# Kernel optimization log

Measured on AMD Instinct MI355X. Metric: run time of the kernel, lower is better.

The kernel has to match this reference:

```python
import jax, jax.numpy as jnp
import numpy as np

N_NODES = 50000
N_HEDGES = 10000
NNZ_INC = 400000
NNZ_E = 80000
NNZ_V = 400000
VDIM = 128
EDIM = 128
OUT_VDIM = 128
OUT_EDIM = 128


def _spmm(rows, cols, vals, X, n_rows):
    # sparse COO [n_rows, n_cols] @ X  -> [n_rows, d]
    return jax.ops.segment_sum(vals[:, None] * X[cols], rows, num_segments=n_rows)


def setup_inputs() -> dict:
    key = jax.random.key(0)
    ks = jax.random.split(key, 20)
    inp = {
        "vfeat": jax.random.normal(ks[0], (N_NODES, VDIM), jnp.float32),
        "efeat": jax.random.normal(ks[1], (N_HEDGES, EDIM), jnp.float32),
        "invDV": jax.random.uniform(ks[2], (N_NODES,), jnp.float32),
        "invDE": jax.random.uniform(ks[3], (N_HEDGES,), jnp.float32),
        "inc_src": jax.random.randint(ks[4], (NNZ_INC,), 0, N_NODES, jnp.int32),
        "inc_dst": jax.random.randint(ks[5], (NNZ_INC,), 0, N_HEDGES, jnp.int32),
        "emat_rows": jax.random.randint(ks[6], (NNZ_E,), 0, N_HEDGES, jnp.int32),
        "emat_cols": jax.random.randint(ks[7], (NNZ_E,), 0, N_HEDGES, jnp.int32),
        "emat_vals": jax.random.normal(ks[8], (NNZ_E,), jnp.float32),
        "vmat_rows": jax.random.randint(ks[9], (NNZ_V,), 0, N_NODES, jnp.int32),
        "vmat_cols": jax.random.randint(ks[10], (NNZ_V,), 0, N_NODES, jnp.int32),
        "vmat_vals": jax.random.normal(ks[11], (NNZ_V,), jnp.float32),
        # parameters (torch Linear: y = x @ W.T + b)
        "Wv": jax.random.normal(ks[12], (OUT_VDIM, VDIM), jnp.float32) * 0.05,
        "We": jax.random.normal(ks[13], (OUT_EDIM, EDIM), jnp.float32) * 0.05,
        "psi1_W": jax.random.normal(ks[14], (VDIM, VDIM + EDIM), jnp.float32) * 0.05,
        "psi1_b": jnp.zeros((VDIM,), jnp.float32),
        "psi2_W": jax.random.normal(ks[15], (EDIM, OUT_VDIM + EDIM), jnp.float32) * 0.05,
        "psi2_b": jnp.zeros((EDIM,), jnp.float32),
    }
    return inp


def reference(vfeat, efeat, invDV, invDE, inc_src, inc_dst,
              emat_rows, emat_cols, emat_vals,
              vmat_rows, vmat_cols, vmat_vals,
              Wv, We, psi1_W, psi1_b, psi2_W, psi2_b):
    N = vfeat.shape[0]
    E = efeat.shape[0]
    # --- 'in' update_all with psi1: per-incidence concat -> linear -> *invDV[src] -> sum into hyperedge
    x = jnp.concatenate([vfeat[inc_src], efeat[inc_dst]], axis=1)  # [nnz, VDIM+EDIM]
    x = x @ psi1_W.T + psi1_b                                       # [nnz, VDIM]
    x = x * invDV[inc_src][:, None]
    A = jax.ops.segment_sum(x, inc_dst, num_segments=E)             # [E, VDIM]
    A = _spmm(emat_rows, emat_cols, emat_vals, A, E)
    _efeat = A + efeat
    # --- 'con' update_all: node gathers sum of incident hyperedge feats
    _vfeat = jax.ops.segment_sum(_efeat[inc_dst], inc_src, num_segments=N)
    vfeat_out = jax.nn.relu(_vfeat @ Wv.T)                           # [N, OUT_VDIM]
    # --- 'in' update_all with psi2 (dv = ones)
    x2 = jnp.concatenate([vfeat_out[inc_src], efeat[inc_dst]], axis=1)
    x2 = x2 @ psi2_W.T + psi2_b                                      # [nnz, EDIM]
    B = jax.ops.segment_sum(x2, inc_dst, num_segments=E) * invDE[:, None]
    # --- 'con' pass with efeat, then vMat spmm, then 'in' sum back to hyperedges
    _vfeat2 = jax.ops.segment_sum(efeat[inc_dst], inc_src, num_segments=N)
    _vfeat2 = _spmm(vmat_rows, vmat_cols, vmat_vals, _vfeat2, N)
    _efeat2 = jax.ops.segment_sum(_vfeat2[inc_src], inc_dst, num_segments=E)
    _efeat2 = _efeat2 + B
    efeat_out = jax.nn.relu(_efeat2 @ We.T)                          # [E, OUT_EDIM]
    return vfeat_out, efeat_out
```

## Files before the change

### kernel.cpp

```cpp
#include <hip/hip_runtime.h>

#define NN 50000
#define NE 10000
#define NNZ_INC 400000
#define NNZ_E 80000
#define NNZ_V 400000
#define D 128
#define KC 32

#define CAP_D 112
#define CAP_S 40
#define CAP_E 40
#define CAP_V 40

#define NE_SH (NE / 8)
#define NN_SH (NN / 8)

#define GN_ 782
#define GE_ 157
#define G_HINC ((NNZ_INC + 255) / 256)
#define G_HIST8 (8 * G_HINC)
#define G_EV ((NNZ_E + NNZ_V + 255) / 256)
#define G_CVTN 6250
#define G_CVTE 1250
#define G_NR16 (NN / 16)
#define G_ER16 (NE / 16)

typedef unsigned short u16;
typedef unsigned int u32;

__device__ __forceinline__ u16 f2bf(float x) {
    unsigned u = __float_as_uint(x);
    unsigned r = u + 0x7fffu + ((u >> 16) & 1u);
    return (u16)(r >> 16);
}
__device__ __forceinline__ float bf2f(u16 h) {
    return __uint_as_float(((unsigned)h) << 16);
}

__device__ __forceinline__ void acc8(uint4 u, float acc[8]) {
    acc[0] += __uint_as_float(u.x << 16);
    acc[1] += __uint_as_float(u.x & 0xffff0000u);
    acc[2] += __uint_as_float(u.y << 16);
    acc[3] += __uint_as_float(u.y & 0xffff0000u);
    acc[4] += __uint_as_float(u.z << 16);
    acc[5] += __uint_as_float(u.z & 0xffff0000u);
    acc[6] += __uint_as_float(u.w << 16);
    acc[7] += __uint_as_float(u.w & 0xffff0000u);
}
__device__ __forceinline__ void fma8(uint4 u, float v, float acc[8]) {
    acc[0] = fmaf(v, __uint_as_float(u.x << 16), acc[0]);
    acc[1] = fmaf(v, __uint_as_float(u.x & 0xffff0000u), acc[1]);
    acc[2] = fmaf(v, __uint_as_float(u.y << 16), acc[2]);
    acc[3] = fmaf(v, __uint_as_float(u.y & 0xffff0000u), acc[3]);
    acc[4] = fmaf(v, __uint_as_float(u.z << 16), acc[4]);
    acc[5] = fmaf(v, __uint_as_float(u.z & 0xffff0000u), acc[5]);
    acc[6] = fmaf(v, __uint_as_float(u.w << 16), acc[6]);
    acc[7] = fmaf(v, __uint_as_float(u.w & 0xffff0000u), acc[7]);
}
__device__ __forceinline__ uint4 pack_bf8(const float acc[8]) {
    uint4 o;
    o.x = (u32)f2bf(acc[0]) | ((u32)f2bf(acc[1]) << 16);
    o.y = (u32)f2bf(acc[2]) | ((u32)f2bf(acc[3]) << 16);
    o.z = (u32)f2bf(acc[4]) | ((u32)f2bf(acc[5]) << 16);
    o.w = (u32)f2bf(acc[6]) | ((u32)f2bf(acc[7]) << 16);
    return o;
}

__device__ __forceinline__ void gemm_acc(
    int bx, const float* __restrict__ X, const float* __restrict__ W, int ldw,
    int M, float acc[8][4])
{
    __shared__ float XsT[KC][68];
    __shared__ float Ws[KC][132];
    const int tid = threadIdx.x;
    const int tx = tid & 31, ty = tid >> 5;
    const int row0 = bx * 64;
    const int c0 = tx * 4;
    const int r0 = ty * 8;

#pragma unroll
    for (int r = 0; r < 8; ++r)
#pragma unroll
        for (int c = 0; c < 4; ++c) acc[r][c] = 0.f;

    for (int kc = 0; kc < D; kc += KC) {
        __syncthreads();
#pragma unroll
        for (int it = 0; it < 2; ++it) {
            int l = tid + it * 256;
            int r = l >> 3, k4 = l & 7;
            float4 v = make_float4(0.f, 0.f, 0.f, 0.f);
            int row = row0 + r;
            if (row < M) v = ((const float4*)(X + (size_t)row * D + kc))[k4];
            int k = k4 * 4;
            XsT[k + 0][r] = v.x; XsT[k + 1][r] = v.y;
            XsT[k + 2][r] = v.z; XsT[k + 3][r] = v.w;
        }
#pragma unroll
        for (int it = 0; it < 4; ++it) {
            int l = tid + it * 256;
            int o = l >> 3, k4 = l & 7;
            float4 w = ((const float4*)(W + (size_t)o * ldw + kc))[k4];
            int k = k4 * 4;
            Ws[k + 0][o] = w.x; Ws[k + 1][o] = w.y;
            Ws[k + 2][o] = w.z; Ws[k + 3][o] = w.w;
        }
        __syncthreads();
#pragma unroll
        for (int k = 0; k < KC; ++k) {
            const float4 a0 = *(const float4*)&XsT[k][r0];
            const float4 a1 = *(const float4*)&XsT[k][r0 + 4];
            const float4 b  = *(const float4*)&Ws[k][c0];
            float av[8] = {a0.x, a0.y, a0.z, a0.w, a1.x, a1.y, a1.z, a1.w};
            float bv[4] = {b.x, b.y, b.z, b.w};
#pragma unroll
            for (int r = 0; r < 8; ++r)
#pragma unroll
                for (int c = 0; c < 4; ++c)
                    acc[r][c] = fmaf(av[r], bv[c], acc[r][c]);
        }
    }
}

__device__ __forceinline__ void gemm_acc2(
    int bx, const float* __restrict__ X1, const float* __restrict__ X2,
    const float* __restrict__ rsf,
    const float* __restrict__ W, int M, float acc[8][4])
{
    __shared__ float XsT[KC][68];
    __shared__ float Ws[KC][132];
    const int tid = threadIdx.x;
    const int tx = tid & 31, ty = tid >> 5;
    const int row0 = bx * 64;
    const int c0 = tx * 4;
    const int r0 = ty * 8;

#pragma unroll
    for (int r = 0; r < 8; ++r)
#pragma unroll
        for (int c = 0; c < 4; ++c) acc[r][c] = 0.f;

    for (int kc = 0; kc < 2 * D; kc += KC) {
        __syncthreads();
        const bool second = (kc >= D);
        const float* Xp = second ? X2 : X1;
        const int kk = second ? kc - D : kc;
#pragma unroll
        for (int it = 0; it < 2; ++it) {
            int l = tid + it * 256;
            int r = l >> 3, k4 = l & 7;
            float4 v = make_float4(0.f, 0.f, 0.f, 0.f);
            int row = row0 + r;
            if (row < M) {
                v = ((const float4*)(Xp + (size_t)row * D + kk))[k4];
                if (second) {
                    float sc = rsf[row];
                    v.x *= sc; v.y *= sc; v.z *= sc; v.w *= sc;
                }
            }
            int k = k4 * 4;
            XsT[k + 0][r] = v.x; XsT[k + 1][r] = v.y;
            XsT[k + 2][r] = v.z; XsT[k + 3][r] = v.w;
        }
#pragma unroll
        for (int it = 0; it < 4; ++it) {
            int l = tid + it * 256;
            int o = l >> 3, k4 = l & 7;
            float4 w = ((const float4*)(W + (size_t)o * (2 * D) + kc))[k4];
            int k = k4 * 4;
            Ws[k + 0][o] = w.x; Ws[k + 1][o] = w.y;
            Ws[k + 2][o] = w.z; Ws[k + 3][o] = w.w;
        }
        __syncthreads();
#pragma unroll
        for (int k = 0; k < KC; ++k) {
            const float4 a0 = *(const float4*)&XsT[k][r0];
            const float4 a1 = *(const float4*)&XsT[k][r0 + 4];
            const float4 b  = *(const float4*)&Ws[k][c0];
            float av[8] = {a0.x, a0.y, a0.z, a0.w, a1.x, a1.y, a1.z, a1.w};
            float bv[4] = {b.x, b.y, b.z, b.w};
#pragma unroll
            for (int r = 0; r < 8; ++r)
#pragma unroll
                for (int c = 0; c < 4; ++c)
                    acc[r][c] = fmaf(av[r], bv[c], acc[r][c]);
        }
    }
}

__global__ __launch_bounds__(256) void mega0(
    const int* __restrict__ inc_src, const int* __restrict__ inc_dst,
    int* __restrict__ cnt_dst, int* __restrict__ cnt_src,
    u16* __restrict__ ell_d, u16* __restrict__ ell_s,
    const float* __restrict__ efeat, const float* __restrict__ vfeat,
    const float* __restrict__ invDV,
    u16* __restrict__ vfi_b, u16* __restrict__ efeat_b)
{
    int b = blockIdx.x;
    if (b < G_HIST8) {
        int shard = b & 7;
        int i = (b >> 3) * 256 + threadIdx.x;
        if (i < NNZ_INC) {
            int s = inc_src[i], d = inc_dst[i];
            if ((u32)(d - shard * NE_SH) < (u32)NE_SH) {
                int rd = atomicAdd(cnt_dst + d, 1);
                if (rd < CAP_D) ell_d[d * CAP_D + rd] = (u16)s;
            }
            if ((u32)(s - shard * NN_SH) < (u32)NN_SH) {
                int rs = atomicAdd(cnt_src + s, 1);
                if (rs < CAP_S) ell_s[s * CAP_S + rs] = (u16)d;
            }
        }
    } else if (b < G_HIST8 + G_CVTN) {
        int i = ((b - G_HIST8) * 256 + threadIdx.x) * 4;
        int row = i >> 7;
        float s = invDV[row];
        float4 v = *(const float4*)(vfeat + i);
        ushort4 u;
        u.x = f2bf(v.x * s); u.y = f2bf(v.y * s);
        u.z = f2bf(v.z * s); u.w = f2bf(v.w * s);
        *(ushort4*)(vfi_b + i) = u;
    } else {
        int i = ((b - G_HIST8 - G_CVTN) * 256 + threadIdx.x) * 4;
        float4 v = *(const float4*)(efeat + i);
        ushort4 u;
        u.x = f2bf(v.x); u.y = f2bf(v.y); u.z = f2bf(v.z); u.w = f2bf(v.w);
        *(ushort4*)(efeat_b + i) = u;
    }
}

__device__ __forceinline__ void segsum_bf_ell16(int rb,
    const int* __restrict__ cnt, int cap, const u16* __restrict__ ell,
    const u16* __restrict__ Tb, u16* __restrict__ Yb, int R)
{
    int r = rb * 16 + (threadIdx.x >> 4);
    int q = threadIdx.x & 15;
    if (r >= R) return;
    int m = min(cnt[r], cap);
    const u16* lst = ell + (size_t)r * cap;
    float acc[8] = {0.f, 0.f, 0.f, 0.f, 0.f, 0.f, 0.f, 0.f};
    int j = 0;
    for (; j + 3 < m; j += 4) {
        ushort4 ix = *(const ushort4*)(lst + j);
        uint4 u0 = *(const uint4*)(Tb + (size_t)ix.x * D + q * 8);
        uint4 u1 = *(const uint4*)(Tb + (size_t)ix.y * D + q * 8);
        uint4 u2 = *(const uint4*)(Tb + (size_t)ix.z * D + q * 8);
        uint4 u3 = *(const uint4*)(Tb + (size_t)ix.w * D + q * 8);
        acc8(u0, acc); acc8(u1, acc); acc8(u2, acc); acc8(u3, acc);
    }
    for (; j < m; ++j) {
        uint4 u0 = *(const uint4*)(Tb + (size_t)lst[j] * D + q * 8);
        acc8(u0, acc);
    }
    ((uint4*)(Yb + (size_t)r * D))[q] = pack_bf8(acc);
}

__device__ __forceinline__ void segsum_f_ell16(int rb,
    const int* __restrict__ cnt, int cap, const u16* __restrict__ ell,
    const u16* __restrict__ Tb, float* __restrict__ Y, int R)
{
    int r = rb * 16 + (threadIdx.x >> 4);
    int q = threadIdx.x & 15;
    if (r >= R) return;
    int m = min(cnt[r], cap);
    const u16* lst = ell + (size_t)r * cap;
    float acc[8] = {0.f, 0.f, 0.f, 0.f, 0.f, 0.f, 0.f, 0.f};
    int j = 0;
    for (; j + 3 < m; j += 4) {
        ushort4 ix = *(const ushort4*)(lst + j);
        uint4 u0 = *(const uint4*)(Tb + (size_t)ix.x * D + q * 8);
        uint4 u1 = *(const uint4*)(Tb + (size_t)ix.y * D + q * 8);
        uint4 u2 = *(const uint4*)(Tb + (size_t)ix.z * D + q * 8);
        uint4 u3 = *(const uint4*)(Tb + (size_t)ix.w * D + q * 8);
        acc8(u0, acc); acc8(u1, acc); acc8(u2, acc); acc8(u3, acc);
    }
    for (; j < m; ++j) {
        uint4 u0 = *(const uint4*)(Tb + (size_t)lst[j] * D + q * 8);
        acc8(u0, acc);
    }
    float* yr = Y + (size_t)r * D;
    ((float4*)yr)[2 * q + 0] = make_float4(acc[0], acc[1], acc[2], acc[3]);
    ((float4*)yr)[2 * q + 1] = make_float4(acc[4], acc[5], acc[6], acc[7]);
}

__device__ __forceinline__ void spmm_bf_ell16(int rb,
    const int* __restrict__ cnt, int cap, const u32* __restrict__ ell,
    const u16* __restrict__ Xb, const float* __restrict__ addend,
    u16* __restrict__ Yb, int R)
{
    int r = rb * 16 + (threadIdx.x >> 4);
    int q = threadIdx.x & 15;
    if (r >= R) return;
    int m = min(cnt[r], cap);
    const u32* lst = ell + (size_t)r * cap;
    float acc[8];
    if (addend) {
        const float* ar = addend + (size_t)r * D;
        float4 lo = ((const float4*)ar)[2 * q + 0];
        float4 hi = ((const float4*)ar)[2 * q + 1];
        acc[0] = lo.x; acc[1] = lo.y; acc[2] = lo.z; acc[3] = lo.w;
        acc[4] = hi.x; acc[5] = hi.y; acc[6] = hi.z; acc[7] = hi.w;
    } else {
#pragma unroll
        for (int i = 0; i < 8; ++i) acc[i] = 0.f;
    }
    int j = 0;
    for (; j + 3 < m; j += 4) {
        uint4 e = *(const uint4*)(lst + j);
        uint4 x0 = *(const uint4*)(Xb + (size_t)(e.x >> 16) * D + q * 8);
        uint4 x1 = *(const uint4*)(Xb + (size_t)(e.y >> 16) * D + q * 8);
        uint4 x2 = *(const uint4*)(Xb + (size_t)(e.z >> 16) * D + q * 8);
        uint4 x3 = *(const uint4*)(Xb + (size_t)(e.w >> 16) * D + q * 8);
        fma8(x0, __uint_as_float(e.x << 16), acc);
        fma8(x1, __uint_as_float(e.y << 16), acc);
        fma8(x2, __uint_as_float(e.z << 16), acc);
        fma8(x3, __uint_as_float(e.w << 16), acc);
    }
    for (; j < m; ++j) {
        u32 e = lst[j];
        uint4 x = *(const uint4*)(Xb + (size_t)(e >> 16) * D + q * 8);
        fma8(x, __uint_as_float(e << 16), acc);
    }
    ((uint4*)(Yb + (size_t)r * D))[q] = pack_bf8(acc);
}

__global__ __launch_bounds__(256) void fusedA(
    const int* __restrict__ erows, const int* __restrict__ ecols,
    const float* __restrict__ evals, int* __restrict__ cnt_e, u32* __restrict__ ev_e,
    const int* __restrict__ vrows, const int* __restrict__ vcols,
    const float* __restrict__ vvals, int* __restrict__ cnt_v, u32* __restrict__ ev_v,
    const float* __restrict__ efeat,
    const float* __restrict__ psi2_W, const float* __restrict__ psi2_b, float* __restrict__ QeP,
    const int* __restrict__ cnt_dst, const u16* __restrict__ ell_d,
    const float* __restrict__ invDV, const u16* __restrict__ vfi_b,
    float* __restrict__ sva, float* __restrict__ wsum,
    const int* __restrict__ cnt_src, const u16* __restrict__ ell_s,
    const u16* __restrict__ efeat_b, u16* __restrict__ vf2_b)
{
    int b = blockIdx.x;
    if (b < G_EV) {
        int i = b * 256 + threadIdx.x;
        if (i < NNZ_E) {
            int r = erows[i];
            int re = atomicAdd(cnt_e + r, 1);
            if (re < CAP_E)
                ev_e[r * CAP_E + re] = ((u32)ecols[i] << 16) | (u32)f2bf(evals[i]);
        } else if (i < NNZ_E + NNZ_V) {
            int j = i - NNZ_E;
            int r = vrows[j];
            int rv = atomicAdd(cnt_v + r, 1);
            if (rv < CAP_V)
                ev_v[r * CAP_V + rv] = ((u32)vcols[j] << 16) | (u32)f2bf(vvals[j]);
        }
    } else if (b < G_EV + GE_) {
        int bx = b - G_EV;
        float acc[8][4];
        gemm_acc(bx, efeat, psi2_W + D, 2 * D, NE, acc);
        int tx = threadIdx.x & 31, ty = threadIdx.x >> 5;
        float4 b4 = ((const float4*)psi2_b)[tx];
#pragma unroll
        for (int r = 0; r < 8; ++r) {
            int row = bx * 64 + ty * 8 + r;
            if (row < NE) {
                float4 v = make_float4(acc[r][0] + b4.x, acc[r][1] + b4.y,
                                       acc[r][2] + b4.z, acc[r][3] + b4.w);
                ((float4*)(QeP + (size_t)row * D))[tx] = v;
            }
        }
    } else if (b < G_EV + GE_ + G_ER16) {
        int e = (b - G_EV - GE_) * 16 + (threadIdx.x >> 4);
        int q = threadIdx.x & 15;
        if (e >= NE) return;
        int m = min(cnt_dst[e], CAP_D);
        const u16* lst = ell_d + (size_t)e * CAP_D;
        float acc[8] = {0.f, 0.f, 0.f, 0.f, 0.f, 0.f, 0.f, 0.f};
        float ws = 0.f;
        int j = 0;
        for (; j + 3 < m; j += 4) {
            ushort4 ix = *(const ushort4*)(lst + j);
            uint4 u0 = *(const uint4*)(vfi_b + (size_t)ix.x * D + q * 8);
            uint4 u1 = *(const uint4*)(vfi_b + (size_t)ix.y * D + q * 8);
            uint4 u2 = *(const uint4*)(vfi_b + (size_t)ix.z * D + q * 8);
            uint4 u3 = *(const uint4*)(vfi_b + (size_t)ix.w * D + q * 8);
            ws += (invDV[ix.x] + invDV[ix.y]) + (invDV[ix.z] + invDV[ix.w]);
            acc8(u0, acc); acc8(u1, acc); acc8(u2, acc); acc8(u3, acc);
        }
        for (; j < m; ++j) {
            int s = lst[j];
            uint4 u0 = *(const uint4*)(vfi_b + (size_t)s * D + q * 8);
            ws += invDV[s];
            acc8(u0, acc);
        }
        float* yr = sva + (size_t)e * D;
        ((float4*)yr)[2 * q + 0] = make_float4(acc[0], acc[1], acc[2], acc[3]);
        ((float4*)yr)[2 * q + 1] = make_float4(acc[4], acc[5], acc[6], acc[7]);
        if (q == 0) wsum[e] = ws;
    } else {
        segsum_bf_ell16(b - G_EV - GE_ - G_ER16, cnt_src, CAP_S, ell_s, efeat_b, vf2_b, NN);
    }
}

__global__ __launch_bounds__(256) void fusedB2(
    const float* __restrict__ sva, const float* __restrict__ efeat,
    const float* __restrict__ wsum,
    const float* __restrict__ psi1_W, const float* __restrict__ psi1_b,
    u16* __restrict__ A_b,
    const int* __restrict__ cnt_v, const u32* __restrict__ ev_v,
    const u16* __restrict__ vf2_b, u16* __restrict__ vf2b_b)
{
    int b = blockIdx.x;
    if (b < GE_) {
        float acc[8][4];
        gemm_acc2(b, sva, efeat, wsum, psi1_W, NE, acc);
        int tx = threadIdx.x & 31, ty = threadIdx.x >> 5;
        float4 b4 = ((const float4*)psi1_b)[tx];
#pragma unroll
        for (int r = 0; r < 8; ++r) {
            int row = b * 64 + ty * 8 + r;
            if (row < NE) {
                float ws = wsum[row];
                ushort4 u;
                u.x = f2bf(fmaf(ws, b4.x, acc[r][0]));
                u.y = f2bf(fmaf(ws, b4.y, acc[r][1]));
                u.z = f2bf(fmaf(ws, b4.z, acc[r][2]));
                u.w = f2bf(fmaf(ws, b4.w, acc[r][3]));
                ((ushort4*)(A_b + (size_t)row * D))[tx] = u;
            }
        }
    } else {
        spmm_bf_ell16(b - GE_, cnt_v, CAP_V, ev_v, vf2_b, nullptr, vf2b_b, NN);
    }
}

__global__ __launch_bounds__(256) void fusedC2(
    const int* __restrict__ cnt_e, const u32* __restrict__ ev_e,
    const u16* __restrict__ A_b, const float* __restrict__ efeat, u16* __restrict__ A2_b,
    const int* __restrict__ cnt_dst, const u16* __restrict__ ell_d,
    const u16* __restrict__ vf2b_b, float* __restrict__ av)
{
    int b = blockIdx.x;
    if (b < G_ER16) spmm_bf_ell16(b, cnt_e, CAP_E, ev_e, A_b, efeat, A2_b, NE);
    else segsum_f_ell16(b - G_ER16, cnt_dst, CAP_D, ell_d, vf2b_b, av, NE);
}

__global__ __launch_bounds__(256) void fusedD2(
    const int* __restrict__ cnt_src, const u16* __restrict__ ell_s,
    const u16* __restrict__ A2_b, float* __restrict__ vf1)
{
    segsum_f_ell16(blockIdx.x, cnt_src, CAP_S, ell_s, A2_b, vf1, NN);
}

__global__ __launch_bounds__(256) void gemmC2_k(
    const float* __restrict__ vf1, const float* __restrict__ Wv,
    const float* __restrict__ psi2_W,
    float* __restrict__ out_v, u16* __restrict__ Z_b)
{
    __shared__ float T[D][68];
    float acc[8][4];
    gemm_acc(blockIdx.x, vf1, Wv, D, NN, acc);
    const int tx = threadIdx.x & 31, ty = threadIdx.x >> 5;
    const int bx = blockIdx.x;
#pragma unroll
    for (int r = 0; r < 8; ++r) {
        int row = bx * 64 + ty * 8 + r;
        float4 v = make_float4(fmaxf(acc[r][0], 0.f), fmaxf(acc[r][1], 0.f),
                               fmaxf(acc[r][2], 0.f), fmaxf(acc[r][3], 0.f));
        if (row < NN) ((float4*)(out_v + (size_t)row * D))[tx] = v;
        int lr = ty * 8 + r;
        T[tx * 4 + 0][lr] = v.x;
        T[tx * 4 + 1][lr] = v.y;
        T[tx * 4 + 2][lr] = v.z;
        T[tx * 4 + 3][lr] = v.w;
    }
    __shared__ float Ws2[KC][132];
    float acc2[8][4];
#pragma unroll
    for (int r = 0; r < 8; ++r)
#pragma unroll
        for (int c = 0; c < 4; ++c) acc2[r][c] = 0.f;
    const int c0 = tx * 4, r0 = ty * 8;
    for (int kc = 0; kc < D; kc += KC) {
        __syncthreads();
#pragma unroll
        for (int it = 0; it < 4; ++it) {
            int l = threadIdx.x + it * 256;
            int o = l >> 3, k4 = l & 7;
            float4 w = ((const float4*)(psi2_W + (size_t)o * (2 * D) + kc))[k4];
            int k = k4 * 4;
            Ws2[k + 0][o] = w.x; Ws2[k + 1][o] = w.y;
            Ws2[k + 2][o] = w.z; Ws2[k + 3][o] = w.w;
        }
        __syncthreads();
#pragma unroll
        for (int k = 0; k < KC; ++k) {
            const float4 a0 = *(const float4*)&T[kc + k][r0];
            const float4 a1 = *(const float4*)&T[kc + k][r0 + 4];
            const float4 bb = *(const float4*)&Ws2[k][c0];
            float avv[8] = {a0.x, a0.y, a0.z, a0.w, a1.x, a1.y, a1.z, a1.w};
            float bv[4] = {bb.x, bb.y, bb.z, bb.w};
#pragma unroll
            for (int r = 0; r < 8; ++r)
#pragma unroll
                for (int c = 0; c < 4; ++c)
                    acc2[r][c] = fmaf(avv[r], bv[c], acc2[r][c]);
        }
    }
#pragma unroll
    for (int r = 0; r < 8; ++r) {
        int row = bx * 64 + ty * 8 + r;
        if (row < NN) {
            ushort4 u;
            u.x = f2bf(acc2[r][0]); u.y = f2bf(acc2[r][1]);
            u.z = f2bf(acc2[r][2]); u.w = f2bf(acc2[r][3]);
            ((ushort4*)(Z_b + (size_t)row * D))[tx] = u;
        }
    }
}

__global__ __launch_bounds__(256) void gatherZ_k(
    const int* __restrict__ cnt_dst, const u16* __restrict__ ell_d,
    const u16* __restrict__ Z_b,
    const float* __restrict__ QeP, const float* __restrict__ invDE,
    const float* __restrict__ av, float* __restrict__ ef2)
{
    int r = blockIdx.x * 16 + (threadIdx.x >> 4);
    int q = threadIdx.x & 15;
    if (r >= NE) return;
    int cd = cnt_dst[r];
    int m = min(cd, CAP_D);
    const u16* lst = ell_d + (size_t)r * CAP_D;
    float acc[8] = {0.f, 0.f, 0.f, 0.f, 0.f, 0.f, 0.f, 0.f};
    int j = 0;
    for (; j + 3 < m; j += 4) {
        ushort4 ix = *(const ushort4*)(lst + j);
        uint4 u0 = *(const uint4*)(Z_b + (size_t)ix.x * D + q * 8);
        uint4 u1 = *(const uint4*)(Z_b + (size_t)ix.y * D + q * 8);
        uint4 u2 = *(const uint4*)(Z_b + (size_t)ix.z * D + q * 8);
        uint4 u3 = *(const uint4*)(Z_b + (size_t)ix.w * D + q * 8);
        acc8(u0, acc); acc8(u1, acc); acc8(u2, acc); acc8(u3, acc);
    }
    for (; j < m; ++j) {
        uint4 u0 = *(const uint4*)(Z_b + (size_t)lst[j] * D + q * 8);
        acc8(u0, acc);
    }
    float deg = (float)cd;
    float ide = invDE[r];
    const float* qp = QeP + (size_t)r * D;
    const float* ap = av + (size_t)r * D;
    float4 q0 = ((const float4*)qp)[2 * q + 0];
    float4 q1 = ((const float4*)qp)[2 * q + 1];
    float4 a0 = ((const float4*)ap)[2 * q + 0];
    float4 a1 = ((const float4*)ap)[2 * q + 1];
    float4 o0, o1;
    o0.x = fmaf(deg, q0.x, acc[0]) * ide + a0.x;
    o0.y = fmaf(deg, q0.y, acc[1]) * ide + a0.y;
    o0.z = fmaf(deg, q0.z, acc[2]) * ide + a0.z;
    o0.w = fmaf(deg, q0.w, acc[3]) * ide + a0.w;
    o1.x = fmaf(deg, q1.x, acc[4]) * ide + a1.x;
    o1.y = fmaf(deg, q1.y, acc[5]) * ide + a1.y;
    o1.z = fmaf(deg, q1.z, acc[6]) * ide + a1.z;
    o1.w = fmaf(deg, q1.w, acc[7]) * ide + a1.w;
    float* yr = ef2 + (size_t)r * D;
    ((float4*)yr)[2 * q + 0] = o0;
    ((float4*)yr)[2 * q + 1] = o1;
}

__global__ __launch_bounds__(256) void gemmE_k(
    const float* __restrict__ ef2, const float* __restrict__ We,
    float* __restrict__ out_e)
{
    float acc[8][4];
    gemm_acc(blockIdx.x, ef2, We, D, NE, acc);
    int tx = threadIdx.x & 31, ty = threadIdx.x >> 5;
#pragma unroll
    for (int r = 0; r < 8; ++r) {
        int row = blockIdx.x * 64 + ty * 8 + r;
        if (row < NE) {
            float4 v = make_float4(fmaxf(acc[r][0], 0.f), fmaxf(acc[r][1], 0.f),
                                   fmaxf(acc[r][2], 0.f), fmaxf(acc[r][3], 0.f));
            ((float4*)(out_e + (size_t)row * D))[tx] = v;
        }
    }
}

extern "C" void kernel_launch(void* const* d_in, const int* in_sizes, int n_in,
                              void* d_out, int out_size, void* d_ws, size_t ws_size,
                              hipStream_t stream)
{
    (void)in_sizes; (void)n_in; (void)out_size; (void)ws_size;
    const float* vfeat     = (const float*)d_in[0];
    const float* efeat     = (const float*)d_in[1];
    const float* invDV     = (const float*)d_in[2];
    const float* invDE     = (const float*)d_in[3];
    const int*   inc_src   = (const int*)d_in[4];
    const int*   inc_dst   = (const int*)d_in[5];
    const int*   emat_rows = (const int*)d_in[6];
    const int*   emat_cols = (const int*)d_in[7];
    const float* emat_vals = (const float*)d_in[8];
    const int*   vmat_rows = (const int*)d_in[9];
    const int*   vmat_cols = (const int*)d_in[10];
    const float* vmat_vals = (const float*)d_in[11];
    const float* Wv        = (const float*)d_in[12];
    const float* We        = (const float*)d_in[13];
    const float* psi1_W    = (const float*)d_in[14];
    const float* psi1_b    = (const float*)d_in[15];
    const float* psi2_W    = (const float*)d_in[16];
    const float* psi2_b    = (const float*)d_in[17];

    const size_t ND = (size_t)NN * D;
    const size_t ED = (size_t)NE * D;

    char* p = (char*)d_ws;
    auto alloc = [&](size_t bytes) {
        size_t a = (size_t)p; a = (a + 255) & ~(size_t)255;
        p = (char*)a; void* r = (void*)p; p += bytes; return r;
    };
    float* QeP   = (float*)alloc(ED * 4);
    float* vf1   = (float*)alloc(ND * 4);
    float* av    = (float*)alloc(ED * 4);
    float* svbuf = (float*)alloc(ED * 4);
    float* wsum  = (float*)alloc((size_t)NE * 4);
    u16* vfi_b   = (u16*)alloc(ND * 2);
    u16* Z_b     = (u16*)alloc(ND * 2);
    u16* vf2_b   = (u16*)alloc(ND * 2);
    u16* vf2b_b  = (u16*)alloc(ND * 2);
    u16* efeat_b = (u16*)alloc(ED * 2);
    u16* A_b     = (u16*)alloc(ED * 2);
    u16* A2_b    = (u16*)alloc(ED * 2);
    int* cnt_dst = (int*)alloc((size_t)(2 * NE + 2 * NN) * 4);
    int* cnt_src = cnt_dst + NE;
    int* cnt_e   = cnt_src + NN;
    int* cnt_v   = cnt_e + NE;
    u16* ell_d   = (u16*)alloc((size_t)NE * CAP_D * 2);
    u16* ell_s   = (u16*)alloc((size_t)NN * CAP_S * 2);
    u32* ev_e    = (u32*)alloc((size_t)NE * CAP_E * 4);
    u32* ev_v    = (u32*)alloc((size_t)NN * CAP_V * 4);

    float* out_v = (float*)d_out;
    float* out_e = out_v + ND;

    dim3 b256(256);

    hipMemsetAsync(cnt_dst, 0, (size_t)(2 * NE + 2 * NN) * sizeof(int), stream);
    mega0<<<G_HIST8 + G_CVTN + G_CVTE, b256, 0, stream>>>(
        inc_src, inc_dst, cnt_dst, cnt_src, ell_d, ell_s,
        efeat, vfeat, invDV, vfi_b, efeat_b);
    fusedA<<<G_EV + GE_ + G_ER16 + G_NR16, b256, 0, stream>>>(
        emat_rows, emat_cols, emat_vals, cnt_e, ev_e,
        vmat_rows, vmat_cols, vmat_vals, cnt_v, ev_v,
        efeat, psi2_W, psi2_b, QeP,
        cnt_dst, ell_d, invDV, vfi_b, svbuf, wsum,
        cnt_src, ell_s, efeat_b, vf2_b);
    fusedB2<<<GE_ + G_NR16, b256, 0, stream>>>(
        svbuf, efeat, wsum, psi1_W, psi1_b, A_b,
        cnt_v, ev_v, vf2_b, vf2b_b);
    fusedC2<<<G_ER16 + G_ER16, b256, 0, stream>>>(
        cnt_e, ev_e, A_b, efeat, A2_b,
        cnt_dst, ell_d, vf2b_b, av);
    fusedD2<<<G_NR16, b256, 0, stream>>>(cnt_src, ell_s, A2_b, vf1);
    gemmC2_k<<<GN_, b256, 0, stream>>>(vf1, Wv, psi2_W, out_v, Z_b);
    gatherZ_k<<<G_ER16, b256, 0, stream>>>(
        cnt_dst, ell_d, Z_b, QeP, invDE, av, svbuf);
    gemmE_k<<<GE_, b256, 0, stream>>>(svbuf, We, out_e);
}
```

Before: 408.2 us.

## Reorder psi2 linear to apply after hyperedge gather, fuse with We GEMM

```diff
diff --git a/kernel.cpp b/kernel.cpp
--- a/kernel.cpp
+++ b/kernel.cpp
@@ -267,6 +267,20 @@
     const u16* lst = ell + (size_t)r * cap;
     float acc[8] = {0.f, 0.f, 0.f, 0.f, 0.f, 0.f, 0.f, 0.f};
     int j = 0;
+    for (; j + 7 < m; j += 8) {
+        ushort4 ixa = *(const ushort4*)(lst + j);
+        ushort4 ixb = *(const ushort4*)(lst + j + 4);
+        uint4 u0 = *(const uint4*)(Tb + (size_t)ixa.x * D + q * 8);
+        uint4 u1 = *(const uint4*)(Tb + (size_t)ixa.y * D + q * 8);
+        uint4 u2 = *(const uint4*)(Tb + (size_t)ixa.z * D + q * 8);
+        uint4 u3 = *(const uint4*)(Tb + (size_t)ixa.w * D + q * 8);
+        uint4 u4 = *(const uint4*)(Tb + (size_t)ixb.x * D + q * 8);
+        uint4 u5 = *(const uint4*)(Tb + (size_t)ixb.y * D + q * 8);
+        uint4 u6 = *(const uint4*)(Tb + (size_t)ixb.z * D + q * 8);
+        uint4 u7 = *(const uint4*)(Tb + (size_t)ixb.w * D + q * 8);
+        acc8(u0, acc); acc8(u1, acc); acc8(u2, acc); acc8(u3, acc);
+        acc8(u4, acc); acc8(u5, acc); acc8(u6, acc); acc8(u7, acc);
+    }
     for (; j + 3 < m; j += 4) {
         ushort4 ix = *(const ushort4*)(lst + j);
         uint4 u0 = *(const uint4*)(Tb + (size_t)ix.x * D + q * 8);
@@ -451,27 +465,62 @@
     segsum_f_ell16(blockIdx.x, cnt_src, CAP_S, ell_s, A2_b, vf1, NN);
 }
 
-__global__ __launch_bounds__(256) void gemmC2_k(
+__global__ __launch_bounds__(256) void gemmC_k(
     const float* __restrict__ vf1, const float* __restrict__ Wv,
-    const float* __restrict__ psi2_W,
-    float* __restrict__ out_v, u16* __restrict__ Z_b)
+    float* __restrict__ out_v, u16* __restrict__ outv_b)
+{
+    float acc[8][4];
+    gemm_acc(blockIdx.x, vf1, Wv, D, NN, acc);
+    int tx = threadIdx.x & 31, ty = threadIdx.x >> 5;
+#pragma unroll
+    for (int r = 0; r < 8; ++r) {
+        int row = blockIdx.x * 64 + ty * 8 + r;
+        if (row < NN) {
+            float4 v = make_float4(fmaxf(acc[r][0], 0.f), fmaxf(acc[r][1], 0.f),
+                                   fmaxf(acc[r][2], 0.f), fmaxf(acc[r][3], 0.f));
+            ((float4*)(out_v + (size_t)row * D))[tx] = v;
+            ushort4 u;
+            u.x = f2bf(v.x); u.y = f2bf(v.y); u.z = f2bf(v.z); u.w = f2bf(v.w);
+            ((ushort4*)(outv_b + (size_t)row * D))[tx] = u;
+        }
+    }
+}
+
+__global__ __launch_bounds__(256) void gather_sv(
+    const int* __restrict__ cnt_dst, const u16* __restrict__ ell_d,
+    const u16* __restrict__ outv_b, float* __restrict__ sv)
+{
+    segsum_f_ell16(blockIdx.x, cnt_dst, CAP_D, ell_d, outv_b, sv, NE);
+}
+
+__global__ __launch_bounds__(256) void gemmBE_k(
+    const float* __restrict__ sv, const float* __restrict__ psi2_W,
+    const int* __restrict__ cnt_dst, const float* __restrict__ QeP,
+    const float* __restrict__ invDE, const float* __restrict__ av,
+    const float* __restrict__ We, float* __restrict__ out_e)
 {
     __shared__ float T[D][68];
     float acc[8][4];
-    gemm_acc(blockIdx.x, vf1, Wv, D, NN, acc);
+    gemm_acc(blockIdx.x, sv, psi2_W, 2 * D, NE, acc);
     const int tx = threadIdx.x & 31, ty = threadIdx.x >> 5;
     const int bx = blockIdx.x;
 #pragma unroll
     for (int r = 0; r < 8; ++r) {
         int row = bx * 64 + ty * 8 + r;
-        float4 v = make_float4(fmaxf(acc[r][0], 0.f), fmaxf(acc[r][1], 0.f),
-                               fmaxf(acc[r][2], 0.f), fmaxf(acc[r][3], 0.f));
-        if (row < NN) ((float4*)(out_v + (size_t)row * D))[tx] = v;
+        float deg = 0.f, ide = 0.f;
+        float4 qe = make_float4(0.f, 0.f, 0.f, 0.f);
+        float4 a  = make_float4(0.f, 0.f, 0.f, 0.f);
+        if (row < NE) {
+            deg = (float)cnt_dst[row];
+            ide = invDE[row];
+            qe = ((const float4*)(QeP + (size_t)row * D))[tx];
+            a  = ((const float4*)(av  + (size_t)row * D))[tx];
+        }
         int lr = ty * 8 + r;
-        T[tx * 4 + 0][lr] = v.x;
-        T[tx * 4 + 1][lr] = v.y;
-        T[tx * 4 + 2][lr] = v.z;
-        T[tx * 4 + 3][lr] = v.w;
+        T[tx * 4 + 0][lr] = fmaf(deg, qe.x, acc[r][0]) * ide + a.x;
+        T[tx * 4 + 1][lr] = fmaf(deg, qe.y, acc[r][1]) * ide + a.y;
+        T[tx * 4 + 2][lr] = fmaf(deg, qe.z, acc[r][2]) * ide + a.z;
+        T[tx * 4 + 3][lr] = fmaf(deg, qe.w, acc[r][3]) * ide + a.w;
     }
     __shared__ float Ws2[KC][132];
     float acc2[8][4];
@@ -486,7 +535,7 @@
         for (int it = 0; it < 4; ++it) {
             int l = threadIdx.x + it * 256;
             int o = l >> 3, k4 = l & 7;
-            float4 w = ((const float4*)(psi2_W + (size_t)o * (2 * D) + kc))[k4];
+            float4 w = ((const float4*)(We + (size_t)o * D + kc))[k4];
             int k = k4 * 4;
             Ws2[k + 0][o] = w.x; Ws2[k + 1][o] = w.y;
             Ws2[k + 2][o] = w.z; Ws2[k + 3][o] = w.w;
@@ -509,76 +558,9 @@
 #pragma unroll
     for (int r = 0; r < 8; ++r) {
         int row = bx * 64 + ty * 8 + r;
-        if (row < NN) {
-            ushort4 u;
-            u.x = f2bf(acc2[r][0]); u.y = f2bf(acc2[r][1]);
-            u.z = f2bf(acc2[r][2]); u.w = f2bf(acc2[r][3]);
-            ((ushort4*)(Z_b + (size_t)row * D))[tx] = u;
-        }
-    }
-}
-
-__global__ __launch_bounds__(256) void gatherZ_k(
-    const int* __restrict__ cnt_dst, const u16* __restrict__ ell_d,
-    const u16* __restrict__ Z_b,
-    const float* __restrict__ QeP, const float* __restrict__ invDE,
-    const float* __restrict__ av, float* __restrict__ ef2)
-{
-    int r = blockIdx.x * 16 + (threadIdx.x >> 4);
-    int q = threadIdx.x & 15;
-    if (r >= NE) return;
-    int cd = cnt_dst[r];
-    int m = min(cd, CAP_D);
-    const u16* lst = ell_d + (size_t)r * CAP_D;
-    float acc[8] = {0.f, 0.f, 0.f, 0.f, 0.f, 0.f, 0.f, 0.f};
-    int j = 0;
-    for (; j + 3 < m; j += 4) {
-        ushort4 ix = *(const ushort4*)(lst + j);
-        uint4 u0 = *(const uint4*)(Z_b + (size_t)ix.x * D + q * 8);
-        uint4 u1 = *(const uint4*)(Z_b + (size_t)ix.y * D + q * 8);
-        uint4 u2 = *(const uint4*)(Z_b + (size_t)ix.z * D + q * 8);
-        uint4 u3 = *(const uint4*)(Z_b + (size_t)ix.w * D + q * 8);
-        acc8(u0, acc); acc8(u1, acc); acc8(u2, acc); acc8(u3, acc);
-    }
-    for (; j < m; ++j) {
-        uint4 u0 = *(const uint4*)(Z_b + (size_t)lst[j] * D + q * 8);
-        acc8(u0, acc);
-    }
-    float deg = (float)cd;
-    float ide = invDE[r];
-    const float* qp = QeP + (size_t)r * D;
-    const float* ap = av + (size_t)r * D;
-    float4 q0 = ((const float4*)qp)[2 * q + 0];
-    float4 q1 = ((const float4*)qp)[2 * q + 1];
-    float4 a0 = ((const float4*)ap)[2 * q + 0];
-    float4 a1 = ((const float4*)ap)[2 * q + 1];
-    float4 o0, o1;
-    o0.x = fmaf(deg, q0.x, acc[0]) * ide + a0.x;
-    o0.y = fmaf(deg, q0.y, acc[1]) * ide + a0.y;
-    o0.z = fmaf(deg, q0.z, acc[2]) * ide + a0.z;
-    o0.w = fmaf(deg, q0.w, acc[3]) * ide + a0.w;
-    o1.x = fmaf(deg, q1.x, acc[4]) * ide + a1.x;
-    o1.y = fmaf(deg, q1.y, acc[5]) * ide + a1.y;
-    o1.z = fmaf(deg, q1.z, acc[6]) * ide + a1.z;
-    o1.w = fmaf(deg, q1.w, acc[7]) * ide + a1.w;
-    float* yr = ef2 + (size_t)r * D;
-    ((float4*)yr)[2 * q + 0] = o0;
-    ((float4*)yr)[2 * q + 1] = o1;
-}
-
-__global__ __launch_bounds__(256) void gemmE_k(
-    const float* __restrict__ ef2, const float* __restrict__ We,
-    float* __restrict__ out_e)
-{
-    float acc[8][4];
-    gemm_acc(blockIdx.x, ef2, We, D, NE, acc);
-    int tx = threadIdx.x & 31, ty = threadIdx.x >> 5;
-#pragma unroll
-    for (int r = 0; r < 8; ++r) {
-        int row = blockIdx.x * 64 + ty * 8 + r;
         if (row < NE) {
-            float4 v = make_float4(fmaxf(acc[r][0], 0.f), fmaxf(acc[r][1], 0.f),
-                                   fmaxf(acc[r][2], 0.f), fmaxf(acc[r][3], 0.f));
+            float4 v = make_float4(fmaxf(acc2[r][0], 0.f), fmaxf(acc2[r][1], 0.f),
+                                   fmaxf(acc2[r][2], 0.f), fmaxf(acc2[r][3], 0.f));
             ((float4*)(out_e + (size_t)row * D))[tx] = v;
         }
     }
@@ -622,7 +604,7 @@
     float* svbuf = (float*)alloc(ED * 4);
     float* wsum  = (float*)alloc((size_t)NE * 4);
     u16* vfi_b   = (u16*)alloc(ND * 2);
-    u16* Z_b     = (u16*)alloc(ND * 2);
+    u16* outv_b  = (u16*)alloc(ND * 2);
     u16* vf2_b   = (u16*)alloc(ND * 2);
     u16* vf2b_b  = (u16*)alloc(ND * 2);
     u16* efeat_b = (u16*)alloc(ED * 2);
@@ -659,8 +641,7 @@
         cnt_e, ev_e, A_b, efeat, A2_b,
         cnt_dst, ell_d, vf2b_b, av);
     fusedD2<<<G_NR16, b256, 0, stream>>>(cnt_src, ell_s, A2_b, vf1);
-    gemmC2_k<<<GN_, b256, 0, stream>>>(vf1, Wv, psi2_W, out_v, Z_b);
-    gatherZ_k<<<G_ER16, b256, 0, stream>>>(
-        cnt_dst, ell_d, Z_b, QeP, invDE, av, svbuf);
-    gemmE_k<<<GE_, b256, 0, stream>>>(svbuf, We, out_e);
-}
+    gemmC_k<<<GN_, b256, 0, stream>>>(vf1, Wv, out_v, outv_b);
+    gather_sv<<<G_ER16, b256, 0, stream>>>(cnt_dst, ell_d, outv_b, svbuf);
+    gemmBE_k<<<GE_, b256, 0, stream>>>(svbuf, psi2_W, cnt_dst, QeP, invDE, av, We, out_e);
+}
```

Result: faster. 362.5 us (-11.2%).
